# Performance work log

Measured on AMD Instinct MI355X. Metric: run time of the kernel, lower is better.

## Reference

```python
import jax, jax.numpy as jnp
import numpy as np

N = 100_000      # nodes
E = 1_600_000    # edges (avg degree 16)
D = 128          # emb_dim
L = 2            # num_layer
BN_EPS = 1e-5


def setup_inputs() -> dict:
    key = jax.random.key(0)
    ks = jax.random.split(key, 16)
    s = 0.05
    inp = {
        # int inputs
        "x": jax.random.randint(ks[0], (N, 9), 0, 2),
        "z": jax.random.randint(ks[1], (N,), 0, 1000),
        "edge_index": jax.random.randint(ks[2], (2, E), 0, N),
        "edge_attr": jax.random.randint(ks[3], (E, 3), 0, 2),
        # learned params
        "atom_emb": jax.random.normal(ks[4], (9, 119, D), jnp.float32) * s,  # padded stacked AtomEncoder tables
        "z_emb": jax.random.normal(ks[5], (1000, D), jnp.float32) * s,
        "bond_emb": jax.random.normal(ks[6], (L, 3, 6, D), jnp.float32) * s,  # padded BondEncoder tables per layer
        "eps": jnp.zeros((L,), jnp.float32),
        "W1": jax.random.normal(ks[7], (L, D, 2 * D), jnp.float32) * s,
        "b1": jnp.zeros((L, 2 * D), jnp.float32),
        "g1": jnp.ones((L, 2 * D), jnp.float32),
        "be1": jnp.zeros((L, 2 * D), jnp.float32),
        "W2": jax.random.normal(ks[8], (L, 2 * D, D), jnp.float32) * s,
        "b2": jnp.zeros((L, D), jnp.float32),
        "bng": jnp.ones((L, D), jnp.float32),
        "bnb": jnp.zeros((L, D), jnp.float32),
    }
    return inp


def _batchnorm(h, g, b):
    # training-mode BatchNorm1d: batch stats, biased variance
    m = h.mean(axis=0)
    v = h.var(axis=0)
    return (h - m) * jax.lax.rsqrt(v + BN_EPS) * g + b


def _multi_embed(tables, idx):
    # tables: [F, V, D], idx: [N, F] -> sum_f tables[f][idx[:, f]]  -> [N, D]
    return jax.vmap(lambda t, i: t[i], in_axes=(0, 1))(tables, idx).sum(axis=0)


def reference(x, z, edge_index, edge_attr, atom_emb, z_emb, bond_emb, eps,
              W1, b1, g1, be1, W2, b2, bng, bnb):
    src, dst = edge_index[0], edge_index[1]
    # h0 = AtomEncoder(x) + z_embedding(z)
    h = _multi_embed(atom_emb, x) + z_emb[z]
    for l in range(L):
        # GINConv: bond encode -> gather -> relu message -> scatter-add -> MLP
        e_emb = _multi_embed(bond_emb[l], edge_attr)          # [E, D]
        msg = jax.nn.relu(h[src] + e_emb)                      # [E, D]
        agg = jax.ops.segment_sum(msg, dst, num_segments=N)    # [N, D]
        pre = (1.0 + eps[l]) * h + agg
        hid = jax.nn.relu(_batchnorm(pre @ W1[l] + b1[l], g1[l], be1[l]))
        hconv = hid @ W2[l] + b2[l]
        h = _batchnorm(hconv, bng[l], bnb[l])
        if l < L - 1:
            h = jax.nn.relu(h)   # dropout ratio 0 -> identity
    return h
```

## Files before the change

### kernel.cpp

```cpp
#include <hip/hip_runtime.h>

#define D 128
#define BN_EPS 1e-5f
#define NSUB 1024
#define CAP2 2048
#define NCOPY 64

typedef __attribute__((ext_vector_type(8))) short short8;
typedef __attribute__((ext_vector_type(4))) float floatx4;

__device__ __forceinline__ float bf2f(unsigned short u) {
    unsigned int x = ((unsigned int)u) << 16;
    return __builtin_bit_cast(float, x);
}
__device__ __forceinline__ unsigned short f2bf(float f) {
    unsigned int x = __builtin_bit_cast(unsigned int, f);
    x = x + 0x7FFFu + ((x >> 16) & 1u);
    return (unsigned short)(x >> 16);
}
__device__ __forceinline__ int magdiv(unsigned int x, unsigned long long magic) {
    return (int)(((unsigned long long)x * magic) >> 44);
}

__global__ __launch_bounds__(256)
void setup_kernel(const int* __restrict__ x, const int* __restrict__ z,
                  const float* __restrict__ atom_emb, const float* __restrict__ z_emb,
                  unsigned short* __restrict__ hb, int N, int nbNode,
                  const float* __restrict__ bond_emb, float* __restrict__ comb,
                  const float* __restrict__ W1, unsigned short* __restrict__ w1p,
                  const float* __restrict__ W2, unsigned short* __restrict__ w2p) {
    const int b = blockIdx.x;
    const int tid = threadIdx.x;
    if (b < nbNode) {
        int gid = b * 256 + tid;
        int node = gid >> 5;
        if (node >= N) return;
        int d0 = (gid & 31) * 4;
        float4 acc = *(const float4*)(z_emb + (size_t)z[node] * D + d0);
#pragma unroll
        for (int f = 0; f < 9; ++f) {
            int v = x[node * 9 + f];
            const float4 t = *(const float4*)(atom_emb + (size_t)(f * 119 + v) * D + d0);
            acc.x += t.x; acc.y += t.y; acc.z += t.z; acc.w += t.w;
        }
        ushort4 o;
        o.x = f2bf(acc.x); o.y = f2bf(acc.y); o.z = f2bf(acc.z); o.w = f2bf(acc.w);
        *(ushort4*)(hb + (size_t)node * D + d0) = o;
    } else if (b < nbNode + 216) {
        int t = (b - nbNode) * 256 + tid;
        int layer = t / (216 * D);
        int idx = t - layer * (216 * D);
        int c = idx >> 7, d = idx & 127;
        int a0 = c / 36, a1 = (c / 6) % 6, a2 = c % 6;
        const float* bb = bond_emb + (size_t)layer * 3 * 6 * D;
        float v = bb[(0 * 6 + a0) * D + d] + bb[(1 * 6 + a1) * D + d] + bb[(2 * 6 + a2) * D + d];
        comb[(size_t)layer * 216 * D + idx] = v;
    } else {
        int isW2 = (b >= nbNode + 216 + 256);
        int t = (b - nbNode - 216 - (isW2 ? 256 : 0)) * 256 + tid;
        int layer = t >> 15;
        int idx = t & 32767;
        int logN = isW2 ? 7 : 8;
        int NCOLS = 1 << logN;
        int k = idx >> logN, n = idx & (NCOLS - 1);
        int k0 = k >> 5, kq = k & 31, q = kq >> 3, j = kq & 7;
        int tt = n >> 4, ln = n & 15;
        size_t dest = (((size_t)k0 * (NCOLS >> 4) + tt) << 9) + ((q << 4) + ln) * 8 + j;
        const float* W = (isW2 ? W2 : W1) + (size_t)layer * 32768;
        unsigned short* Wp = (isW2 ? w2p : w1p) + (size_t)layer * 32768;
        Wp[dest] = f2bf(W[idx]);
    }
}

__global__ __launch_bounds__(256)
void partition_kernel(const int* __restrict__ ei, const int* __restrict__ ea,
                      unsigned int* __restrict__ subL, int* __restrict__ tail2,
                      int E, int N, unsigned long long magic, int ntiles, int nblocks) {
    __shared__ int lcnt[1024], lbase[1024];
    const int tid = threadIdx.x;
    for (int tile = blockIdx.x; tile < ntiles; tile += nblocks) {
        const int tb = tile * 4096;
#pragma unroll
        for (int i = 0; i < 4; ++i) lcnt[tid + i * 256] = 0;
        __syncthreads();
        int sub[16];
        unsigned int entry[16];
#pragma unroll
        for (int j = 0; j < 16; ++j) {
            int e = tb + j * 256 + tid;
            if (e < E) {
                int dst = ei[E + e];
                int c = (ea[3 * e] * 6 + ea[3 * e + 1]) * 6 + ea[3 * e + 2];
                int k = magdiv((unsigned)dst * 1024u, magic);
                int lo = (int)(((long long)k * N + 1023) >> 10);
                sub[j] = k;
                entry[j] = (unsigned int)ei[e] | ((unsigned int)c << 17) |
                           ((unsigned int)(dst - lo) << 25);
                atomicAdd(&lcnt[k], 1);
            } else {
                sub[j] = -1;
            }
        }
        __syncthreads();
#pragma unroll
        for (int i = 0; i < 4; ++i) {
            int k = tid + i * 256;
            int c = lcnt[k];
            if (c) lbase[k] = atomicAdd(&tail2[k], c);
            lcnt[k] = 0;
        }
        __syncthreads();
#pragma unroll
        for (int j = 0; j < 16; ++j) {
            if (sub[j] >= 0) {
                int k = sub[j];
                int pos = lbase[k] + atomicAdd(&lcnt[k], 1);
                if (pos < CAP2) subL[(size_t)k * CAP2 + pos] = entry[j];
            }
        }
        __syncthreads();
    }
}

__global__ __launch_bounds__(1024)
void subscan_kernel(const int* __restrict__ tail2, int* __restrict__ subbase,
                    int* __restrict__ offsets, int N) {
    const int tid = threadIdx.x, lane = tid & 63, wid = tid >> 6;
    int v = min(tail2[tid], CAP2);
    int s = v;
#pragma unroll
    for (int off = 1; off < 64; off <<= 1) {
        int t = __shfl_up(s, off, 64);
        if (lane >= off) s += t;
    }
    __shared__ int ws[16];
    if (lane == 63) ws[wid] = s;
    __syncthreads();
    if (wid == 0) {
        int w = (lane < 16) ? ws[lane] : 0;
#pragma unroll
        for (int off = 1; off < 16; off <<= 1) {
            int t = __shfl_up(w, off, 64);
            if (lane >= off) w += t;
        }
        if (lane < 16) ws[lane] = w;
    }
    __syncthreads();
    int excl = (wid ? ws[wid - 1] : 0) + s - v;
    subbase[tid] = excl;
    if (tid == 1023) offsets[N] = excl + v;
}

__global__ __launch_bounds__(256)
void csr_sort_kernel(const unsigned int* __restrict__ subL, const int* __restrict__ tail2,
                     const int* __restrict__ subbase, int* __restrict__ offsets,
                     int* __restrict__ bucket, int N) {
    const int k = blockIdx.x;
    const int tid = threadIdx.x, lane = tid & 63, wid = tid >> 6;
    const int len = min(tail2[k], CAP2);
    const int base = subbase[k];
    const int lo = (int)(((long long)k * N + 1023) >> 10);
    const int hi = (int)(((long long)(k + 1) * N + 1023) >> 10);
    const int nn = hi - lo;
    __shared__ int cnt[128], loff[128], wsum[4];
    __shared__ unsigned int sorted[CAP2];
    const unsigned int* src = subL + (size_t)k * CAP2;

    if (tid < 128) cnt[tid] = 0;
    __syncthreads();
    for (int i = tid; i < len; i += 256) atomicAdd(&cnt[src[i] >> 25], 1);
    __syncthreads();
    int v = (tid < 128) ? cnt[tid] : 0;
    int s = v;
#pragma unroll
    for (int off = 1; off < 64; off <<= 1) {
        int t = __shfl_up(s, off, 64);
        if (lane >= off) s += t;
    }
    if (lane == 63) wsum[wid] = s;
    __syncthreads();
    if (tid < 128) loff[tid] = ((wid == 1) ? wsum[0] : 0) + s - v;
    __syncthreads();
    if (tid < nn) offsets[lo + tid] = base + loff[tid];
    if (tid < 128) cnt[tid] = 0;
    __syncthreads();
    for (int i = tid; i < len; i += 256) {
        unsigned int e = src[i];
        int ld = e >> 25;
        int pos = loff[ld] + atomicAdd(&cnt[ld], 1);
        sorted[pos] = e & 0x1FFFFFFu;
    }
    __syncthreads();
    for (int i = tid; i < len; i += 256) bucket[base + i] = (int)sorted[i];
}

__global__ __launch_bounds__(256)
void gather_reduce_kernel(const int* __restrict__ offsets, const int* __restrict__ bucket,
                          const float* __restrict__ comb,
                          const unsigned short* __restrict__ hb,
                          const float* __restrict__ eps_l,
                          unsigned short* __restrict__ pre, int N) {
    int gid = blockIdx.x * blockDim.x + threadIdx.x;
    int node = gid >> 4;
    if (node >= N) return;
    int d0 = (gid & 15) * 8;

    union U8 { int4 i; unsigned short u[8]; };
    union C8 { float4 v[2]; float f[8]; };
    float s = 1.0f + eps_l[0];
    float a[8];
    {
        U8 hv; hv.i = *(const int4*)(hb + (size_t)node * D + d0);
#pragma unroll
        for (int j = 0; j < 8; ++j) a[j] = bf2f(hv.u[j]) * s;
    }
    const int beg = offsets[node], end = offsets[node + 1];
    for (int p = beg; p < end; p += 4) {
        int rem = end - p;
        int pk0 = bucket[p];
        int pk1 = bucket[rem > 1 ? p + 1 : p];
        int pk2 = bucket[rem > 2 ? p + 2 : p];
        int pk3 = bucket[rem > 3 ? p + 3 : p];
        U8 h0, h1, h2, h3;
        C8 c0, c1, c2, c3;
        h0.i = *(const int4*)(hb + (size_t)(pk0 & 0x1FFFF) * D + d0);
        c0.v[0] = *(const float4*)(comb + (size_t)(pk0 >> 17) * D + d0);
        c0.v[1] = *(const float4*)(comb + (size_t)(pk0 >> 17) * D + d0 + 4);
        h1.i = *(const int4*)(hb + (size_t)(pk1 & 0x1FFFF) * D + d0);
        c1.v[0] = *(const float4*)(comb + (size_t)(pk1 >> 17) * D + d0);
        c1.v[1] = *(const float4*)(comb + (size_t)(pk1 >> 17) * D + d0 + 4);
        h2.i = *(const int4*)(hb + (size_t)(pk2 & 0x1FFFF) * D + d0);
        c2.v[0] = *(const float4*)(comb + (size_t)(pk2 >> 17) * D + d0);
        c2.v[1] = *(const float4*)(comb + (size_t)(pk2 >> 17) * D + d0 + 4);
        h3.i = *(const int4*)(hb + (size_t)(pk3 & 0x1FFFF) * D + d0);
        c3.v[0] = *(const float4*)(comb + (size_t)(pk3 >> 17) * D + d0);
        c3.v[1] = *(const float4*)(comb + (size_t)(pk3 >> 17) * D + d0 + 4);
#pragma unroll
        for (int j = 0; j < 8; ++j) a[j] += fmaxf(bf2f(h0.u[j]) + c0.f[j], 0.0f);
        if (rem > 1) {
#pragma unroll
            for (int j = 0; j < 8; ++j) a[j] += fmaxf(bf2f(h1.u[j]) + c1.f[j], 0.0f);
        }
        if (rem > 2) {
#pragma unroll
            for (int j = 0; j < 8; ++j) a[j] += fmaxf(bf2f(h2.u[j]) + c2.f[j], 0.0f);
        }
        if (rem > 3) {
#pragma unroll
            for (int j = 0; j < 8; ++j) a[j] += fmaxf(bf2f(h3.u[j]) + c3.f[j], 0.0f);
        }
    }
    U8 o;
#pragma unroll
    for (int j = 0; j < 8; ++j) o.u[j] = f2bf(a[j]);
    *(int4*)(pre + (size_t)node * D + d0) = o.i;
}

template <int K, int NCOLS, int TRANSFORM>
__global__ __launch_bounds__(256)
void mfma_gemm_kernel(const unsigned short* __restrict__ A,
                      const unsigned short* __restrict__ Wp,
                      const float* __restrict__ bias,
                      const float* __restrict__ tscale, const float* __restrict__ tshift,
                      unsigned short* __restrict__ Cbf,
                      float* __restrict__ gacc, int M) {
    constexpr int NT = NCOLS / 16;
    constexpr int NCHUNK = K / 32;
    constexpr int CPP = NCHUNK / 2;
    constexpr int CTS = NCOLS + 8;
    constexpr int WS_SH = (64 * CTS > 16384) ? 64 * CTS : 16384;
    __shared__ unsigned short Ws[WS_SH];
    __shared__ float red[NCOLS * 2];

    const int tid = threadIdx.x;
    const int wave = tid >> 6, lane = tid & 63;
    const int quad = lane >> 4, ln = lane & 15;
    const int m_base = blockIdx.x * 64 + wave * 16;
    int arow = m_base + ln;
    if (arow >= M) arow = M - 1;
    const int kq = quad * 8;

    int4 araw[NCHUNK];
#pragma unroll
    for (int c = 0; c < NCHUNK; ++c)
        araw[c] = *(const int4*)(A + (size_t)arow * K + c * 32 + kq);

    for (int i = tid; i < NCOLS * 2; i += 256) red[i] = 0.f;

    floatx4 acc[NT];
#pragma unroll
    for (int t = 0; t < NT; ++t) acc[t] = (floatx4){0.f, 0.f, 0.f, 0.f};

#pragma unroll
    for (int ph = 0; ph < 2; ++ph) {
        if (ph) __syncthreads();
#pragma unroll
        for (int i = 0; i < 16384; i += 2048)
            *(int4*)&Ws[i + tid * 8] = *(const int4*)&Wp[ph * 16384 + i + tid * 8];
        __syncthreads();
#pragma unroll
        for (int cc = 0; cc < CPP; ++cc) {
            const int c = ph * CPP + cc;
            short8 afrag;
            if constexpr (TRANSFORM) {
                union { int4 i; unsigned short u[8]; } raw;
                raw.i = araw[c];
                const int kb = c * 32 + kq;
                float4 sc0 = *(const float4*)(tscale + kb);
                float4 sc1 = *(const float4*)(tscale + kb + 4);
                float4 sh0 = *(const float4*)(tshift + kb);
                float4 sh1 = *(const float4*)(tshift + kb + 4);
                union { short8 v; unsigned short u[8]; } au;
                au.u[0] = f2bf(fmaxf(bf2f(raw.u[0]) * sc0.x + sh0.x, 0.f));
                au.u[1] = f2bf(fmaxf(bf2f(raw.u[1]) * sc0.y + sh0.y, 0.f));
                au.u[2] = f2bf(fmaxf(bf2f(raw.u[2]) * sc0.z + sh0.z, 0.f));
                au.u[3] = f2bf(fmaxf(bf2f(raw.u[3]) * sc0.w + sh0.w, 0.f));
                au.u[4] = f2bf(fmaxf(bf2f(raw.u[4]) * sc1.x + sh1.x, 0.f));
                au.u[5] = f2bf(fmaxf(bf2f(raw.u[5]) * sc1.y + sh1.y, 0.f));
                au.u[6] = f2bf(fmaxf(bf2f(raw.u[6]) * sc1.z + sh1.z, 0.f));
                au.u[7] = f2bf(fmaxf(bf2f(raw.u[7]) * sc1.w + sh1.w, 0.f));
                afrag = au.v;
            } else {
                afrag = __builtin_bit_cast(short8, araw[c]);
            }
#pragma unroll
            for (int t = 0; t < NT; ++t) {
                short8 bfrag = *(const short8*)&Ws[(((cc * NT) + t) << 9) + lane * 8];
                acc[t] = __builtin_amdgcn_mfma_f32_16x16x32_bf16(afrag, bfrag, acc[t], 0, 0, 0);
            }
        }
    }

    __syncthreads();
#pragma unroll
    for (int t = 0; t < NT; ++t) {
        int col = t * 16 + ln;
        float bv = bias[col];
        float sv = 0.f, qv = 0.f;
#pragma unroll
        for (int r = 0; r < 4; ++r) {
            int lrow = wave * 16 + quad * 4 + r;
            float v = acc[t][r] + bv;
            Ws[lrow * CTS + col] = f2bf(v);
            if (m_base + quad * 4 + r < M) { sv += v; qv += v * v; }
        }
        sv += __shfl_xor(sv, 16, 64); sv += __shfl_xor(sv, 32, 64);
        qv += __shfl_xor(qv, 16, 64); qv += __shfl_xor(qv, 32, 64);
        if (quad == 0) {
            atomicAdd(&red[col], sv);
            atomicAdd(&red[NCOLS + col], qv);
        }
    }
    __syncthreads();
    {
        constexpr int RI4 = NCOLS / 8;
        const int row0 = blockIdx.x * 64;
        unsigned short* cb = Cbf + (size_t)row0 * NCOLS;
        for (int i = tid; i < 64 * RI4; i += 256) {
            int row = i / RI4, cc = i - row * RI4;
            if (row0 + row < M)
                *(int4*)(cb + (size_t)i * 8) = *(const int4*)&Ws[row * CTS + cc * 8];
        }
    }
    float* gout = gacc + (size_t)(blockIdx.x & (NCOPY - 1)) * (NCOLS * 2);
    for (int i = tid; i < NCOLS * 2; i += 256) atomicAdd(&gout[i], red[i]);
}

template <int NCOLS>
__global__ void stats_final_kernel(float* __restrict__ gacc,
                                   const float* __restrict__ g, const float* __restrict__ b,
                                   float* __restrict__ scale, float* __restrict__ shift,
                                   float invN) {
    int col = threadIdx.x;
    if (col < NCOLS) {
        float s = 0.f, q = 0.f;
        for (int c = 0; c < NCOPY; ++c) {
            float* p = gacc + (size_t)c * (NCOLS * 2);
            s += p[col];
            q += p[NCOLS + col];
            p[col] = 0.f;
            p[NCOLS + col] = 0.f;
        }
        float mean = s * invN;
        float var = q * invN - mean * mean;
        float inv = 1.0f / sqrtf(var + BN_EPS);
        float sc = g[col] * inv;
        scale[col] = sc;
        shift[col] = b[col] - mean * sc;
    }
}

__global__ void bn_apply_kernel(const unsigned short* __restrict__ Xb,
                                float* __restrict__ Yf, unsigned short* __restrict__ Yb,
                                const float* __restrict__ scale, const float* __restrict__ shift,
                                int N, int mode) {
    int gid = blockIdx.x * blockDim.x + threadIdx.x;
    int node = gid >> 5;
    if (node >= N) return;
    int d0 = (gid & 31) * 4;
    ushort4 b = *(const ushort4*)(Xb + (size_t)node * D + d0);
    float4 v;
    v.x = bf2f(b.x); v.y = bf2f(b.y); v.z = bf2f(b.z); v.w = bf2f(b.w);
    float4 sc = *(const float4*)(scale + d0);
    float4 sh = *(const float4*)(shift + d0);
    float4 o;
    o.x = v.x * sc.x + sh.x;
    o.y = v.y * sc.y + sh.y;
    o.z = v.z * sc.z + sh.z;
    o.w = v.w * sc.w + sh.w;
    if (mode == 0) {
        ushort4 ob;
        ob.x = f2bf(fmaxf(o.x, 0.f));
        ob.y = f2bf(fmaxf(o.y, 0.f));
        ob.z = f2bf(fmaxf(o.z, 0.f));
        ob.w = f2bf(fmaxf(o.w, 0.f));
        *(ushort4*)(Yb + (size_t)node * D + d0) = ob;
    } else {
        *(float4*)(Yf + (size_t)node * D + d0) = o;
    }
}

extern "C" void kernel_launch(void* const* d_in, const int* in_sizes, int n_in,
                              void* d_out, int out_size, void* d_ws, size_t ws_size,
                              hipStream_t stream) {
    const int*   x        = (const int*)d_in[0];
    const int*   z        = (const int*)d_in[1];
    const int*   ei       = (const int*)d_in[2];
    const int*   ea       = (const int*)d_in[3];
    const float* atom_emb = (const float*)d_in[4];
    const float* z_emb    = (const float*)d_in[5];
    const float* bond_emb = (const float*)d_in[6];
    const float* eps      = (const float*)d_in[7];
    const float* W1       = (const float*)d_in[8];
    const float* b1       = (const float*)d_in[9];
    const float* g1       = (const float*)d_in[10];
    const float* be1      = (const float*)d_in[11];
    const float* W2       = (const float*)d_in[12];
    const float* b2       = (const float*)d_in[13];
    const float* bng      = (const float*)d_in[14];
    const float* bnb      = (const float*)d_in[15];

    const int N = in_sizes[1];
    const int E = in_sizes[3] / 3;

    float* h = (float*)d_out;

    const int ngb = (N + 63) / 64;
    const unsigned long long magic = ((1ULL << 44) / (unsigned int)N) + 1;

    char* ws = (char*)d_ws;
    size_t off = 0;
    auto alloc = [&](size_t bytes) { void* p = ws + off; off += (bytes + 255) & ~(size_t)255; return p; };
    unsigned short* pre_bf = (unsigned short*)alloc((size_t)N * D * 2);
    unsigned short* out2_bf = pre_bf;
    unsigned short* out1_bf = (unsigned short*)alloc((size_t)N * 2 * D * 2);
    unsigned short* hb      = (unsigned short*)alloc((size_t)N * D * 2);
    int* offsets = (int*)alloc((size_t)(N + 1) * 4);
    int* bucket  = (int*)alloc((size_t)E * 4);
    unsigned int* subL = (unsigned int*)alloc((size_t)NSUB * CAP2 * 4);
    int* subbase = (int*)alloc(NSUB * 4);
    float* stats = (float*)alloc(1024 * 4);
    float* gstats = (float*)alloc(((size_t)NCOPY * 768 + 1024) * 4);
    unsigned short* w1p  = (unsigned short*)alloc((size_t)2 * D * 2 * D * 2);
    unsigned short* w2p  = (unsigned short*)alloc((size_t)2 * 2 * D * D * 2);
    float* comb = (float*)alloc((size_t)2 * 216 * D * 4);

    float* scale1 = stats;
    float* shift1 = stats + 256;
    float* scale2 = stats + 512;
    float* shift2 = stats + 640;
    float* gacc1 = gstats;
    float* gacc2 = gstats + (size_t)NCOPY * 512;
    int* tail2 = (int*)(gstats + (size_t)NCOPY * 768);

    const float invN = 1.0f / (float)N;
    const int ntiles = (E + 4095) / 4096;
    const int nbNode = (N * 32 + 255) / 256;

    hipMemsetAsync(gstats, 0, ((size_t)NCOPY * 768 + 1024) * sizeof(float), stream);
    partition_kernel<<<256, 256, 0, stream>>>(ei, ea, subL, tail2, E, N, magic, ntiles, 256);
    subscan_kernel<<<1, 1024, 0, stream>>>(tail2, subbase, offsets, N);
    csr_sort_kernel<<<NSUB, 256, 0, stream>>>(subL, tail2, subbase, offsets, bucket, N);

    setup_kernel<<<nbNode + 216 + 256 + 256, 256, 0, stream>>>(
        x, z, atom_emb, z_emb, hb, N, nbNode, bond_emb, comb, W1, w1p, W2, w2p);

    for (int l = 0; l < 2; ++l) {
        gather_reduce_kernel<<<(N * 16 + 255) / 256, 256, 0, stream>>>(
            offsets, bucket, comb + (size_t)l * 216 * D, hb, eps + l, pre_bf, N);

        mfma_gemm_kernel<128, 256, 0><<<ngb, 256, 0, stream>>>(
            pre_bf, w1p + (size_t)l * D * 2 * D, b1 + (size_t)l * 2 * D,
            nullptr, nullptr, out1_bf, gacc1, N);
        stats_final_kernel<256><<<1, 256, 0, stream>>>(
            gacc1, g1 + (size_t)l * 2 * D, be1 + (size_t)l * 2 * D, scale1, shift1, invN);

        mfma_gemm_kernel<256, 128, 1><<<ngb, 256, 0, stream>>>(
            out1_bf, w2p + (size_t)l * 2 * D * D, b2 + (size_t)l * D,
            scale1, shift1, out2_bf, gacc2, N);
        stats_final_kernel<128><<<1, 128, 0, stream>>>(
            gacc2, bng + (size_t)l * D, bnb + (size_t)l * D, scale2, shift2, invN);

        bn_apply_kernel<<<(N * 32 + 255) / 256, 256, 0, stream>>>(
            out2_bf, h, hb, scale2, shift2, N, l == 0 ? 0 : 1);
    }
}
```

Baseline: 502.7 us.

## Fold BN stats finalization into consumers and merge sort with setup kernel

Removes the two single-block stats_final kernels per layer. Each consumer (the second GEMM and bn_apply) now reduces the per-copy partial sums and computes scale and shift itself into shared memory. The CSR sort and embedding/weight setup kernels are merged into one launch, and bn_apply becomes a grid-stride loop over fewer blocks. Accumulators are now kept separate per layer, so the in-kernel zeroing is no longer needed. The cost is that every consumer block redundantly reduces 64 copies of the stats, which is extra global reads at the start of each block.

```diff
diff --git a/kernel.cpp b/kernel.cpp
--- a/kernel.cpp
+++ b/kernel.cpp
@@ -23,14 +23,136 @@
 }
 
 __global__ __launch_bounds__(256)
-void setup_kernel(const int* __restrict__ x, const int* __restrict__ z,
-                  const float* __restrict__ atom_emb, const float* __restrict__ z_emb,
-                  unsigned short* __restrict__ hb, int N, int nbNode,
-                  const float* __restrict__ bond_emb, float* __restrict__ comb,
-                  const float* __restrict__ W1, unsigned short* __restrict__ w1p,
-                  const float* __restrict__ W2, unsigned short* __restrict__ w2p) {
-    const int b = blockIdx.x;
+void partition_kernel(const int* __restrict__ ei, const int* __restrict__ ea,
+                      unsigned int* __restrict__ subL, int* __restrict__ tail2,
+                      int E, int N, unsigned long long magic, int ntiles, int nblocks) {
+    __shared__ int lcnt[1024], lbase[1024];
     const int tid = threadIdx.x;
+    for (int tile = blockIdx.x; tile < ntiles; tile += nblocks) {
+        const int tb = tile * 4096;
+#pragma unroll
+        for (int i = 0; i < 4; ++i) lcnt[tid + i * 256] = 0;
+        __syncthreads();
+        int sub[16];
+        unsigned int entry[16];
+#pragma unroll
+        for (int j = 0; j < 16; ++j) {
+            int e = tb + j * 256 + tid;
+            if (e < E) {
+                int dst = ei[E + e];
+                int c = (ea[3 * e] * 6 + ea[3 * e + 1]) * 6 + ea[3 * e + 2];
+                int k = magdiv((unsigned)dst * 1024u, magic);
+                int lo = (int)(((long long)k * N + 1023) >> 10);
+                sub[j] = k;
+                entry[j] = (unsigned int)ei[e] | ((unsigned int)c << 17) |
+                           ((unsigned int)(dst - lo) << 25);
+                atomicAdd(&lcnt[k], 1);
+            } else {
+                sub[j] = -1;
+            }
+        }
+        __syncthreads();
+#pragma unroll
+        for (int i = 0; i < 4; ++i) {
+            int k = tid + i * 256;
+            int c = lcnt[k];
+            if (c) lbase[k] = atomicAdd(&tail2[k], c);
+            lcnt[k] = 0;
+        }
+        __syncthreads();
+#pragma unroll
+        for (int j = 0; j < 16; ++j) {
+            if (sub[j] >= 0) {
+                int k = sub[j];
+                int pos = lbase[k] + atomicAdd(&lcnt[k], 1);
+                if (pos < CAP2) subL[(size_t)k * CAP2 + pos] = entry[j];
+            }
+        }
+        __syncthreads();
+    }
+}
+
+__global__ __launch_bounds__(1024)
+void subscan_kernel(const int* __restrict__ tail2, int* __restrict__ subbase,
+                    int* __restrict__ offsets, int N) {
+    const int tid = threadIdx.x, lane = tid & 63, wid = tid >> 6;
+    int v = min(tail2[tid], CAP2);
+    int s = v;
+#pragma unroll
+    for (int off = 1; off < 64; off <<= 1) {
+        int t = __shfl_up(s, off, 64);
+        if (lane >= off) s += t;
+    }
+    __shared__ int ws[16];
+    if (lane == 63) ws[wid] = s;
+    __syncthreads();
+    if (wid == 0) {
+        int w = (lane < 16) ? ws[lane] : 0;
+#pragma unroll
+        for (int off = 1; off < 16; off <<= 1) {
+            int t = __shfl_up(w, off, 64);
+            if (lane >= off) w += t;
+        }
+        if (lane < 16) ws[lane] = w;
+    }
+    __syncthreads();
+    int excl = (wid ? ws[wid - 1] : 0) + s - v;
+    subbase[tid] = excl;
+    if (tid == 1023) offsets[N] = excl + v;
+}
+
+__global__ __launch_bounds__(256)
+void sort_setup_kernel(const unsigned int* __restrict__ subL, const int* __restrict__ tail2,
+                       const int* __restrict__ subbase, int* __restrict__ offsets,
+                       int* __restrict__ bucket, int N,
+                       const int* __restrict__ x, const int* __restrict__ z,
+                       const float* __restrict__ atom_emb, const float* __restrict__ z_emb,
+                       unsigned short* __restrict__ hb, int nbNode,
+                       const float* __restrict__ bond_emb, float* __restrict__ comb,
+                       const float* __restrict__ W1, unsigned short* __restrict__ w1p,
+                       const float* __restrict__ W2, unsigned short* __restrict__ w2p) {
+    __shared__ int cnt[128], loff[128], wsum[4];
+    __shared__ unsigned int sorted[CAP2];
+    const int tid = threadIdx.x;
+    if (blockIdx.x < NSUB) {
+        const int k = blockIdx.x;
+        const int lane = tid & 63, wid = tid >> 6;
+        const int len = min(tail2[k], CAP2);
+        const int base = subbase[k];
+        const int lo = (int)(((long long)k * N + 1023) >> 10);
+        const int hi = (int)(((long long)(k + 1) * N + 1023) >> 10);
+        const int nn = hi - lo;
+        const unsigned int* src = subL + (size_t)k * CAP2;
+
+        if (tid < 128) cnt[tid] = 0;
+        __syncthreads();
+        for (int i = tid; i < len; i += 256) atomicAdd(&cnt[src[i] >> 25], 1);
+        __syncthreads();
+        int v = (tid < 128) ? cnt[tid] : 0;
+        int s = v;
+#pragma unroll
+        for (int off = 1; off < 64; off <<= 1) {
+            int t = __shfl_up(s, off, 64);
+            if (lane >= off) s += t;
+        }
+        if (lane == 63) wsum[wid] = s;
+        __syncthreads();
+        if (tid < 128) loff[tid] = ((wid == 1) ? wsum[0] : 0) + s - v;
+        __syncthreads();
+        if (tid < nn) offsets[lo + tid] = base + loff[tid];
+        if (tid < 128) cnt[tid] = 0;
+        __syncthreads();
+        for (int i = tid; i < len; i += 256) {
+            unsigned int e = src[i];
+            int ld = e >> 25;
+            int pos = loff[ld] + atomicAdd(&cnt[ld], 1);
+            sorted[pos] = e & 0x1FFFFFFu;
+        }
+        __syncthreads();
+        for (int i = tid; i < len; i += 256) bucket[base + i] = (int)sorted[i];
+        return;
+    }
+    const int b = blockIdx.x - NSUB;
     if (b < nbNode) {
         int gid = b * 256 + tid;
         int node = gid >> 5;
@@ -73,128 +195,6 @@
 }
 
 __global__ __launch_bounds__(256)
-void partition_kernel(const int* __restrict__ ei, const int* __restrict__ ea,
-                      unsigned int* __restrict__ subL, int* __restrict__ tail2,
-                      int E, int N, unsigned long long magic, int ntiles, int nblocks) {
-    __shared__ int lcnt[1024], lbase[1024];
-    const int tid = threadIdx.x;
-    for (int tile = blockIdx.x; tile < ntiles; tile += nblocks) {
-        const int tb = tile * 4096;
-#pragma unroll
-        for (int i = 0; i < 4; ++i) lcnt[tid + i * 256] = 0;
-        __syncthreads();
-        int sub[16];
-        unsigned int entry[16];
-#pragma unroll
-        for (int j = 0; j < 16; ++j) {
-            int e = tb + j * 256 + tid;
-            if (e < E) {
-                int dst = ei[E + e];
-                int c = (ea[3 * e] * 6 + ea[3 * e + 1]) * 6 + ea[3 * e + 2];
-                int k = magdiv((unsigned)dst * 1024u, magic);
-                int lo = (int)(((long long)k * N + 1023) >> 10);
-                sub[j] = k;
-                entry[j] = (unsigned int)ei[e] | ((unsigned int)c << 17) |
-                           ((unsigned int)(dst - lo) << 25);
-                atomicAdd(&lcnt[k], 1);
-            } else {
-                sub[j] = -1;
-            }
-        }
-        __syncthreads();
-#pragma unroll
-        for (int i = 0; i < 4; ++i) {
-            int k = tid + i * 256;
-            int c = lcnt[k];
-            if (c) lbase[k] = atomicAdd(&tail2[k], c);
-            lcnt[k] = 0;
-        }
-        __syncthreads();
-#pragma unroll
-        for (int j = 0; j < 16; ++j) {
-            if (sub[j] >= 0) {
-                int k = sub[j];
-                int pos = lbase[k] + atomicAdd(&lcnt[k], 1);
-                if (pos < CAP2) subL[(size_t)k * CAP2 + pos] = entry[j];
-            }
-        }
-        __syncthreads();
-    }
-}
-
-__global__ __launch_bounds__(1024)
-void subscan_kernel(const int* __restrict__ tail2, int* __restrict__ subbase,
-                    int* __restrict__ offsets, int N) {
-    const int tid = threadIdx.x, lane = tid & 63, wid = tid >> 6;
-    int v = min(tail2[tid], CAP2);
-    int s = v;
-#pragma unroll
-    for (int off = 1; off < 64; off <<= 1) {
-        int t = __shfl_up(s, off, 64);
-        if (lane >= off) s += t;
-    }
-    __shared__ int ws[16];
-    if (lane == 63) ws[wid] = s;
-    __syncthreads();
-    if (wid == 0) {
-        int w = (lane < 16) ? ws[lane] : 0;
-#pragma unroll
-        for (int off = 1; off < 16; off <<= 1) {
-            int t = __shfl_up(w, off, 64);
-            if (lane >= off) w += t;
-        }
-        if (lane < 16) ws[lane] = w;
-    }
-    __syncthreads();
-    int excl = (wid ? ws[wid - 1] : 0) + s - v;
-    subbase[tid] = excl;
-    if (tid == 1023) offsets[N] = excl + v;
-}
-
-__global__ __launch_bounds__(256)
-void csr_sort_kernel(const unsigned int* __restrict__ subL, const int* __restrict__ tail2,
-                     const int* __restrict__ subbase, int* __restrict__ offsets,
-                     int* __restrict__ bucket, int N) {
-    const int k = blockIdx.x;
-    const int tid = threadIdx.x, lane = tid & 63, wid = tid >> 6;
-    const int len = min(tail2[k], CAP2);
-    const int base = subbase[k];
-    const int lo = (int)(((long long)k * N + 1023) >> 10);
-    const int hi = (int)(((long long)(k + 1) * N + 1023) >> 10);
-    const int nn = hi - lo;
-    __shared__ int cnt[128], loff[128], wsum[4];
-    __shared__ unsigned int sorted[CAP2];
-    const unsigned int* src = subL + (size_t)k * CAP2;
-
-    if (tid < 128) cnt[tid] = 0;
-    __syncthreads();
-    for (int i = tid; i < len; i += 256) atomicAdd(&cnt[src[i] >> 25], 1);
-    __syncthreads();
-    int v = (tid < 128) ? cnt[tid] : 0;
-    int s = v;
-#pragma unroll
-    for (int off = 1; off < 64; off <<= 1) {
-        int t = __shfl_up(s, off, 64);
-        if (lane >= off) s += t;
-    }
-    if (lane == 63) wsum[wid] = s;
-    __syncthreads();
-    if (tid < 128) loff[tid] = ((wid == 1) ? wsum[0] : 0) + s - v;
-    __syncthreads();
-    if (tid < nn) offsets[lo + tid] = base + loff[tid];
-    if (tid < 128) cnt[tid] = 0;
-    __syncthreads();
-    for (int i = tid; i < len; i += 256) {
-        unsigned int e = src[i];
-        int ld = e >> 25;
-        int pos = loff[ld] + atomicAdd(&cnt[ld], 1);
-        sorted[pos] = e & 0x1FFFFFFu;
-    }
-    __syncthreads();
-    for (int i = tid; i < len; i += 256) bucket[base + i] = (int)sorted[i];
-}
-
-__global__ __launch_bounds__(256)
 void gather_reduce_kernel(const int* __restrict__ offsets, const int* __restrict__ bucket,
                           const float* __restrict__ comb,
                           const unsigned short* __restrict__ hb,
@@ -261,7 +261,9 @@
 void mfma_gemm_kernel(const unsigned short* __restrict__ A,
                       const unsigned short* __restrict__ Wp,
                       const float* __restrict__ bias,
-                      const float* __restrict__ tscale, const float* __restrict__ tshift,
+                      const float* __restrict__ gaccP,
+                      const float* __restrict__ gam, const float* __restrict__ bet,
+                      float invN,
                       unsigned short* __restrict__ Cbf,
                       float* __restrict__ gacc, int M) {
     constexpr int NT = NCOLS / 16;
@@ -271,6 +273,7 @@
     constexpr int WS_SH = (64 * CTS > 16384) ? 64 * CTS : 16384;
     __shared__ unsigned short Ws[WS_SH];
     __shared__ float red[NCOLS * 2];
+    __shared__ float tsc_s[TRANSFORM ? K : 1], tsh_s[TRANSFORM ? K : 1];
 
     const int tid = threadIdx.x;
     const int wave = tid >> 6, lane = tid & 63;
@@ -287,6 +290,23 @@
 
     for (int i = tid; i < NCOLS * 2; i += 256) red[i] = 0.f;
 
+    if constexpr (TRANSFORM) {
+        for (int col = tid; col < K; col += 256) {
+            float s = 0.f, q = 0.f;
+            for (int c = 0; c < NCOPY; ++c) {
+                const float* p = gaccP + (size_t)c * (K * 2);
+                s += p[col];
+                q += p[K + col];
+            }
+            float mean = s * invN;
+            float var = q * invN - mean * mean;
+            float inv = 1.0f / sqrtf(var + BN_EPS);
+            float sc = gam[col] * inv;
+            tsc_s[col] = sc;
+            tsh_s[col] = bet[col] - mean * sc;
+        }
+    }
+
     floatx4 acc[NT];
 #pragma unroll
     for (int t = 0; t < NT; ++t) acc[t] = (floatx4){0.f, 0.f, 0.f, 0.f};
@@ -306,10 +326,10 @@
                 union { int4 i; unsigned short u[8]; } raw;
                 raw.i = araw[c];
                 const int kb = c * 32 + kq;
-                float4 sc0 = *(const float4*)(tscale + kb);
-                float4 sc1 = *(const float4*)(tscale + kb + 4);
-                float4 sh0 = *(const float4*)(tshift + kb);
-                float4 sh1 = *(const float4*)(tshift + kb + 4);
+                float4 sc0 = *(const float4*)&tsc_s[kb];
+                float4 sc1 = *(const float4*)&tsc_s[kb + 4];
+                float4 sh0 = *(const float4*)&tsh_s[kb];
+                float4 sh1 = *(const float4*)&tsh_s[kb + 4];
                 union { short8 v; unsigned short u[8]; } au;
                 au.u[0] = f2bf(fmaxf(bf2f(raw.u[0]) * sc0.x + sh0.x, 0.f));
                 au.u[1] = f2bf(fmaxf(bf2f(raw.u[1]) * sc0.y + sh0.y, 0.f));
@@ -366,57 +386,54 @@
     for (int i = tid; i < NCOLS * 2; i += 256) atomicAdd(&gout[i], red[i]);
 }
 
-template <int NCOLS>
-__global__ void stats_final_kernel(float* __restrict__ gacc,
-                                   const float* __restrict__ g, const float* __restrict__ b,
-                                   float* __restrict__ scale, float* __restrict__ shift,
-                                   float invN) {
-    int col = threadIdx.x;
-    if (col < NCOLS) {
+__global__ __launch_bounds__(256)
+void bn_apply_kernel(const unsigned short* __restrict__ Xb,
+                     float* __restrict__ Yf, unsigned short* __restrict__ Yb,
+                     const float* __restrict__ gacc,
+                     const float* __restrict__ g, const float* __restrict__ b,
+                     float invN, int N, int mode, int nblocks) {
+    __shared__ float sc_s[D], sh_s[D];
+    const int tid = threadIdx.x;
+    if (tid < D) {
         float s = 0.f, q = 0.f;
         for (int c = 0; c < NCOPY; ++c) {
-            float* p = gacc + (size_t)c * (NCOLS * 2);
-            s += p[col];
-            q += p[NCOLS + col];
-            p[col] = 0.f;
-            p[NCOLS + col] = 0.f;
+            const float* p = gacc + (size_t)c * (D * 2);
+            s += p[tid];
+            q += p[D + tid];
         }
         float mean = s * invN;
         float var = q * invN - mean * mean;
         float inv = 1.0f / sqrtf(var + BN_EPS);
-        float sc = g[col] * inv;
-        scale[col] = sc;
-        shift[col] = b[col] - mean * sc;
-    }
-}
-
-__global__ void bn_apply_kernel(const unsigned short* __restrict__ Xb,
-                                float* __restrict__ Yf, unsigned short* __restrict__ Yb,
-                                const float* __restrict__ scale, const float* __restrict__ shift,
-                                int N, int mode) {
-    int gid = blockIdx.x * blockDim.x + threadIdx.x;
-    int node = gid >> 5;
-    if (node >= N) return;
-    int d0 = (gid & 31) * 4;
-    ushort4 b = *(const ushort4*)(Xb + (size_t)node * D + d0);
-    float4 v;
-    v.x = bf2f(b.x); v.y = bf2f(b.y); v.z = bf2f(b.z); v.w = bf2f(b.w);
-    float4 sc = *(const float4*)(scale + d0);
-    float4 sh = *(const float4*)(shift + d0);
-    float4 o;
-    o.x = v.x * sc.x + sh.x;
-    o.y = v.y * sc.y + sh.y;
-    o.z = v.z * sc.z + sh.z;
-    o.w = v.w * sc.w + sh.w;
-    if (mode == 0) {
-        ushort4 ob;
-        ob.x = f2bf(fmaxf(o.x, 0.f));
-        ob.y = f2bf(fmaxf(o.y, 0.f));
-        ob.z = f2bf(fmaxf(o.z, 0.f));
-        ob.w = f2bf(fmaxf(o.w, 0.f));
-        *(ushort4*)(Yb + (size_t)node * D + d0) = ob;
-    } else {
-        *(float4*)(Yf + (size_t)node * D + d0) = o;
+        float sc = g[tid] * inv;
+        sc_s[tid] = sc;
+        sh_s[tid] = b[tid] - mean * sc;
+    }
+    __syncthreads();
+    const int nchunk = (N + 7) / 8;
+    const int d0 = (tid & 31) * 4;
+    for (int chunk = blockIdx.x; chunk < nchunk; chunk += nblocks) {
+        int node = chunk * 8 + (tid >> 5);
+        if (node >= N) continue;
+        ushort4 xb = *(const ushort4*)(Xb + (size_t)node * D + d0);
+        float4 v;
+        v.x = bf2f(xb.x); v.y = bf2f(xb.y); v.z = bf2f(xb.z); v.w = bf2f(xb.w);
+        float4 sc = *(const float4*)&sc_s[d0];
+        float4 sh = *(const float4*)&sh_s[d0];
+        float4 o;
+        o.x = v.x * sc.x + sh.x;
+        o.y = v.y * sc.y + sh.y;
+        o.z = v.z * sc.z + sh.z;
+        o.w = v.w * sc.w + sh.w;
+        if (mode == 0) {
+            ushort4 ob;
+            ob.x = f2bf(fmaxf(o.x, 0.f));
+            ob.y = f2bf(fmaxf(o.y, 0.f));
+            ob.z = f2bf(fmaxf(o.z, 0.f));
+            ob.w = f2bf(fmaxf(o.w, 0.f));
+            *(ushort4*)(Yb + (size_t)node * D + d0) = ob;
+        } else {
+            *(float4*)(Yf + (size_t)node * D + d0) = o;
+        }
     }
 }
 
@@ -459,49 +476,45 @@
     int* bucket  = (int*)alloc((size_t)E * 4);
     unsigned int* subL = (unsigned int*)alloc((size_t)NSUB * CAP2 * 4);
     int* subbase = (int*)alloc(NSUB * 4);
-    float* stats = (float*)alloc(1024 * 4);
-    float* gstats = (float*)alloc(((size_t)NCOPY * 768 + 1024) * 4);
+    float* gstats = (float*)alloc(((size_t)NCOPY * 1536 + 1024) * 4);
     unsigned short* w1p  = (unsigned short*)alloc((size_t)2 * D * 2 * D * 2);
     unsigned short* w2p  = (unsigned short*)alloc((size_t)2 * 2 * D * D * 2);
     float* comb = (float*)alloc((size_t)2 * 216 * D * 4);
 
-    float* scale1 = stats;
-    float* shift1 = stats + 256;
-    float* scale2 = stats + 512;
-    float* shift2 = stats + 640;
-    float* gacc1 = gstats;
-    float* gacc2 = gstats + (size_t)NCOPY * 512;
-    int* tail2 = (int*)(gstats + (size_t)NCOPY * 768);
+    float* gacc1base = gstats;
+    float* gacc2base = gstats + (size_t)2 * NCOPY * 512;
+    int* tail2 = (int*)(gstats + (size_t)NCOPY * 1536);
 
     const float invN = 1.0f / (float)N;
     const int ntiles = (E + 4095) / 4096;
     const int nbNode = (N * 32 + 255) / 256;
-
-    hipMemsetAsync(gstats, 0, ((size_t)NCOPY * 768 + 1024) * sizeof(float), stream);
+    const int nbBN = (N + 63) / 64;
+
+    hipMemsetAsync(gstats, 0, ((size_t)NCOPY * 1536 + 1024) * sizeof(float), stream);
     partition_kernel<<<256, 256, 0, stream>>>(ei, ea, subL, tail2, E, N, magic, ntiles, 256);
     subscan_kernel<<<1, 1024, 0, stream>>>(tail2, subbase, offsets, N);
-    csr_sort_kernel<<<NSUB, 256, 0, stream>>>(subL, tail2, subbase, offsets, bucket, N);
-
-    setup_kernel<<<nbNode + 216 + 256 + 256, 256, 0, stream>>>(
-        x, z, atom_emb, z_emb, hb, N, nbNode, bond_emb, comb, W1, w1p, W2, w2p);
+    sort_setup_kernel<<<NSUB + nbNode + 216 + 512, 256, 0, stream>>>(
+        subL, tail2, subbase, offsets, bucket, N,
+        x, z, atom_emb, z_emb, hb, nbNode, bond_emb, comb, W1, w1p, W2, w2p);
 
     for (int l = 0; l < 2; ++l) {
+        float* gacc1 = gacc1base + (size_t)l * NCOPY * 512;
+        float* gacc2 = gacc2base + (size_t)l * NCOPY * 256;
+
         gather_reduce_kernel<<<(N * 16 + 255) / 256, 256, 0, stream>>>(
             offsets, bucket, comb + (size_t)l * 216 * D, hb, eps + l, pre_bf, N);
 
         mfma_gemm_kernel<128, 256, 0><<<ngb, 256, 0, stream>>>(
             pre_bf, w1p + (size_t)l * D * 2 * D, b1 + (size_t)l * 2 * D,
-            nullptr, nullptr, out1_bf, gacc1, N);
-        stats_final_kernel<256><<<1, 256, 0, stream>>>(
-            gacc1, g1 + (size_t)l * 2 * D, be1 + (size_t)l * 2 * D, scale1, shift1, invN);
+            nullptr, nullptr, nullptr, invN, out1_bf, gacc1, N);
 
         mfma_gemm_kernel<256, 128, 1><<<ngb, 256, 0, stream>>>(
             out1_bf, w2p + (size_t)l * 2 * D * D, b2 + (size_t)l * D,
-            scale1, shift1, out2_bf, gacc2, N);
-        stats_final_kernel<128><<<1, 128, 0, stream>>>(
-            gacc2, bng + (size_t)l * D, bnb + (size_t)l * D, scale2, shift2, invN);
-
-        bn_apply_kernel<<<(N * 32 + 255) / 256, 256, 0, stream>>>(
-            out2_bf, h, hb, scale2, shift2, N, l == 0 ? 0 : 1);
-    }
-}
+            gacc1, g1 + (size_t)l * 2 * D, be1 + (size_t)l * 2 * D, invN,
+            out2_bf, gacc2, N);
+
+        bn_apply_kernel<<<nbBN, 256, 0, stream>>>(
+            out2_bf, h, hb, gacc2, bng + (size_t)l * D, bnb + (size_t)l * D,
+            invN, N, l == 0 ? 0 : 1, nbBN);
+    }
+}
```

After: 483.7 us. 3.8% less time.
